# Optimization experiments

Hardware: AMD Instinct MI355X
Metric: run time of the kernel (lower is better)

The kernel has to match this reference:

```python
import jax, jax.numpy as jnp
import numpy as np

NUM_HEADS = 16


def setup_inputs() -> dict:
    key = jax.random.key(0)
    k1, k2, k3, k4 = jax.random.split(key, 4)
    B, N, C = 4, 2048, 1024
    x = jax.random.normal(k1, (B, N, C), dtype=jnp.float32)
    g_info = jax.random.normal(k2, (2, 4, C), dtype=jnp.float32)
    qkv_w = jax.random.normal(k3, (3 * C, C), dtype=jnp.float32) * 0.02
    proj_w = jax.random.normal(k4, (C, C), dtype=jnp.float32) * 0.02
    proj_b = jnp.zeros((C,), dtype=jnp.float32)
    return {"x": x, "g_info": g_info, "qkv_w": qkv_w, "proj_w": proj_w, "proj_b": proj_b}


def reference(x, g_info, qkv_w, proj_w, proj_b):
    B, N, C = x.shape
    H = NUM_HEADS
    D = C // H
    scale = D ** -0.5
    # qkv projection (no bias): [B,N,3C] -> [B,N,3,H,D]
    qkv = (x @ qkv_w.T).reshape(B, N, 3, H, D)
    q, k, v = qkv[:, :, 0], qkv[:, :, 1], qkv[:, :, 2]  # each [B,N,H,D]
    # global-info fusion: g_info[0] -> (4,H,D); rows = q_g, k_g, v_g, t_g
    gl = g_info[0].reshape(4, H, D)
    q_g = gl[0][None, None]  # [1,1,H,D]
    k_g = gl[1][None, None]
    # NOTE: source computes min/max rescaled q_g/k_g but they are dead code;
    # the attention actually uses the unscaled additive fusion below.
    q_fused = q + q_g
    k_fused = k + k_g
    # memory_efficient_attention(q,k,v): softmax(q k^T / sqrt(D)) v
    attn = jnp.einsum("bqhd,bkhd->bhqk", q_fused, k_fused) * scale
    attn = jax.nn.softmax(attn, axis=-1)
    out = jnp.einsum("bhqk,bkhd->bqhd", attn, v).reshape(B, N, C)
    out = out @ proj_w.T + proj_b
    return (out, g_info[1:])
```

## Files before the change

### kernel.cpp

```cpp
#include <hip/hip_runtime.h>

typedef _Float16 h4 __attribute__((ext_vector_type(4)));
typedef _Float16 h8 __attribute__((ext_vector_type(8)));
typedef __fp16 fp16x2 __attribute__((ext_vector_type(2)));
typedef float f4 __attribute__((ext_vector_type(4)));
typedef float f16v __attribute__((ext_vector_type(16)));

#define MFMA16(a,b,c) __builtin_amdgcn_mfma_f32_16x16x32_f16(a, b, c, 0, 0, 0)
#define MFMA32(a,b,c) __builtin_amdgcn_mfma_f32_32x32x16_f16(a, b, c, 0, 0, 0)
#define EXP2(x) __builtin_amdgcn_exp2f(x)

__device__ __forceinline__ void gload_lds16(const _Float16* g, _Float16* l) {
    __builtin_amdgcn_global_load_lds((const __attribute__((address_space(1))) void*)g,
                                     (__attribute__((address_space(3))) void*)l, 16, 0, 0);
}

__device__ __forceinline__ h8 ldfrag_sw(const _Float16* S, int R, int kk, int kq) {
    int b = kk * 4 + (kq >> 1);
    int o = (kq & 1) * 4;
    const _Float16* base = S + R * 64;
    h4 lo = *(const h4*)(base + ((b ^ (R & 7)) * 8) + o);
    h4 hi = *(const h4*)(base + (((b + 2) ^ (R & 7)) * 8) + o);
    return __builtin_shufflevector(lo, hi, 0, 1, 2, 3, 4, 5, 6, 7);
}

__device__ __forceinline__ void gemm_main(const _Float16* __restrict__ A, const _Float16* __restrict__ B,
                                          int K, int tM, int tN, int tid,
                                          _Float16* As, _Float16* Bs, f4 acc[4][4]) {
    int lane = tid & 63, w = tid >> 6;
    int wm = w >> 1, wn = w & 1;
    int ln = lane & 15, kq = lane >> 4;
    int r = tid >> 3;
    int sb = tid & 7;

    for (int k0 = 0; k0 < K; k0 += 64) {
#pragma unroll
        for (int it = 0; it < 4; ++it) {
            int row = r + it * 32;
            int srcb = sb ^ (row & 7);
            const _Float16* ga = A + (size_t)(tM * 128 + row) * K + k0 + srcb * 8;
            const _Float16* gb = B + (size_t)(tN * 128 + row) * K + k0 + srcb * 8;
            _Float16* la = As + ((tid & ~63) + it * 256) * 8;
            _Float16* lb = Bs + ((tid & ~63) + it * 256) * 8;
            gload_lds16(ga, la);
            gload_lds16(gb, lb);
        }
        __syncthreads();
#pragma unroll
        for (int kk = 0; kk < 2; ++kk) {
            h8 af[4], bf[4];
#pragma unroll
            for (int mi = 0; mi < 4; ++mi) af[mi] = ldfrag_sw(As, wm * 64 + mi * 16 + ln, kk, kq);
#pragma unroll
            for (int ni = 0; ni < 4; ++ni) bf[ni] = ldfrag_sw(Bs, wn * 64 + ni * 16 + ln, kk, kq);
#pragma unroll
            for (int mi = 0; mi < 4; ++mi)
#pragma unroll
                for (int ni = 0; ni < 4; ++ni) acc[mi][ni] = MFMA16(af[mi], bf[ni], acc[mi][ni]);
        }
        __syncthreads();
    }
}

__global__ __launch_bounds__(256) void k_cvt(const float* __restrict__ in, _Float16* __restrict__ out, int n8) {
    int stride = gridDim.x * blockDim.x;
    for (int i = blockIdx.x * blockDim.x + threadIdx.x; i < n8; i += stride) {
        float4 a = ((const float4*)in)[i * 2];
        float4 b = ((const float4*)in)[i * 2 + 1];
        h8 r = {(_Float16)a.x, (_Float16)a.y, (_Float16)a.z, (_Float16)a.w,
                (_Float16)b.x, (_Float16)b.y, (_Float16)b.z, (_Float16)b.w};
        ((h8*)out)[i] = r;
    }
}

__global__ __launch_bounds__(256) void k_qkv(const _Float16* __restrict__ A, const _Float16* __restrict__ B,
                                             const float* __restrict__ g, _Float16* __restrict__ Qf,
                                             _Float16* __restrict__ Kf, _Float16* __restrict__ Vt) {
    __shared__ __align__(16) _Float16 As[128 * 64];
    __shared__ __align__(16) _Float16 Bs[128 * 64];
    int tid = threadIdx.x;
    int tN = blockIdx.x, tM = blockIdx.y;
    int lane = tid & 63, w = tid >> 6;
    int wm = w >> 1, wn = w & 1;
    int ln = lane & 15, kq = lane >> 4;

    f4 acc[4][4] = {};
    gemm_main(A, B, 1024, tM, tN, tid, As, Bs, acc);

#pragma unroll
    for (int mi = 0; mi < 4; ++mi) {
#pragma unroll
        for (int ni = 0; ni < 4; ++ni) {
#pragma unroll
            for (int r = 0; r < 4; ++r) {
                int gr = tM * 128 + wm * 64 + mi * 16 + kq * 4 + r;
                int gc = tN * 128 + wn * 64 + ni * 16 + ln;
                float val = acc[mi][ni][r];
                int which = gc >> 10;
                int c = gc & 1023, h = c >> 6, d = c & 63;
                int b = gr >> 11, n = gr & 2047;
                int bh = b * 16 + h;
                if (which == 0) {
                    val += g[c];
                    Qf[((size_t)bh * 2048 + n) * 64 + d] = (_Float16)val;
                } else if (which == 1) {
                    val += g[1024 + c];
                    Kf[((size_t)bh * 2048 + n) * 64 + d] = (_Float16)val;
                } else {
                    Vt[((size_t)bh * 64 + d) * 2048 + n] = (_Float16)val;
                }
            }
        }
    }
}

__global__ __launch_bounds__(256) void k_attn(const _Float16* __restrict__ Qf, const _Float16* __restrict__ Kf,
                                              const _Float16* __restrict__ Vt, _Float16* __restrict__ Oa) {
    __shared__ __align__(16) _Float16 Kl[64 * 64];
    __shared__ __align__(16) _Float16 Vl[64 * 64];
    int tid = threadIdx.x;
    int qt = blockIdx.x, bh = blockIdx.y;
    int lane = tid & 63, w = tid >> 6;
    int l31 = lane & 31, hi = lane >> 5;
    const _Float16* Qb = Qf + (size_t)bh * 2048 * 64;
    const _Float16* Kb = Kf + (size_t)bh * 2048 * 64;
    const _Float16* Vb = Vt + (size_t)bh * 64 * 2048;
    int qrow0 = qt * 128 + w * 32;

    h8 qfr[4];
#pragma unroll
    for (int dc = 0; dc < 4; ++dc) {
        h8 t = *(const h8*)(Qb + (size_t)(qrow0 + l31) * 64 + dc * 16 + hi * 8);
#pragma unroll
        for (int j = 0; j < 8; ++j) t[j] = (_Float16)((float)t[j] * 0.18033688f);
        qfr[dc] = t;
    }

    f16v o0 = {}, o1 = {};
    float m_run = -1e30f, l_run = 0.f;

    for (int kv0 = 0; kv0 < 2048; kv0 += 64) {
#pragma unroll
        for (int it = 0; it < 2; ++it) {
            int slot = tid + it * 256;
            int row = slot >> 3, blk = slot & 7;
            int sb = (blk ^ (row & 7)) * 8;
            *(uint4*)&Kl[row * 64 + sb] = *(const uint4*)(Kb + (size_t)(kv0 + row) * 64 + blk * 8);
            *(uint4*)&Vl[row * 64 + sb] = *(const uint4*)(Vb + (size_t)row * 2048 + kv0 + blk * 8);
        }
        __syncthreads();

        f16v s0 = {}, s1 = {};
        int sw = l31 & 7;
#pragma unroll
        for (int dc = 0; dc < 4; ++dc) {
            int cb = dc * 2 + hi;
            h8 kf0 = *(const h8*)&Kl[l31 * 64 + ((cb ^ sw) * 8)];
            h8 kf1 = *(const h8*)&Kl[(32 + l31) * 64 + ((cb ^ sw) * 8)];
            s0 = MFMA32(kf0, qfr[dc], s0);
            s1 = MFMA32(kf1, qfr[dc], s1);
        }

        float pmax = -1e30f;
#pragma unroll
        for (int r = 0; r < 16; ++r) pmax = fmaxf(pmax, fmaxf(s0[r], s1[r]));
        pmax = fmaxf(pmax, __shfl_xor(pmax, 32, 64));

        bool ok = (pmax <= m_run + 11.5f);
        if (!__all(ok)) {
            float mnew = fmaxf(m_run, pmax);
            float alpha = EXP2(m_run - mnew);
            m_run = mnew;
            l_run *= alpha;
#pragma unroll
            for (int r = 0; r < 16; ++r) {
                int src = (r & 3) + 8 * (r >> 2) + 4 * hi;
                float a = __shfl(alpha, src, 64);
                o0[r] *= a;
                o1[r] *= a;
            }
        }

        float ps0[16], ps1[16];
        float psum = 0.f;
#pragma unroll
        for (int r = 0; r < 16; ++r) { ps0[r] = EXP2(s0[r] - m_run); psum += ps0[r]; }
#pragma unroll
        for (int r = 0; r < 16; ++r) { ps1[r] = EXP2(s1[r] - m_run); psum += ps1[r]; }
        psum += __shfl_xor(psum, 32, 64);
        l_run += psum;

        unsigned W[16];
#pragma unroll
        for (int i = 0; i < 8; ++i) {
            union { fp16x2 h; unsigned u; } a, b;
            a.h = __builtin_amdgcn_cvt_pkrtz(ps0[2 * i], ps0[2 * i + 1]);
            b.h = __builtin_amdgcn_cvt_pkrtz(ps1[2 * i], ps1[2 * i + 1]);
            W[i] = a.u;
            W[8 + i] = b.u;
        }

#pragma unroll
        for (int t = 0; t < 2; ++t) {
#pragma unroll
            for (int kcl = 0; kcl < 2; ++kcl) {
                unsigned w0 = W[t * 8 + kcl * 4 + 0], w1 = W[t * 8 + kcl * 4 + 1];
                unsigned w2 = W[t * 8 + kcl * 4 + 2], w3 = W[t * 8 + kcl * 4 + 3];
                asm("v_permlane32_swap_b32 %0, %1" : "+v"(w0), "+v"(w2));
                asm("v_permlane32_swap_b32 %0, %1" : "+v"(w1), "+v"(w3));
                union { unsigned u[4]; h8 v; } pf;
                pf.u[0] = w0; pf.u[1] = w1; pf.u[2] = w2; pf.u[3] = w3;
                int cb = (t * 2 + kcl) * 2 + hi;
                h8 vf0 = *(const h8*)&Vl[l31 * 64 + ((cb ^ sw) * 8)];
                h8 vf1 = *(const h8*)&Vl[(32 + l31) * 64 + ((cb ^ sw) * 8)];
                o0 = MFMA32(pf.v, vf0, o0);
                o1 = MFMA32(pf.v, vf1, o1);
            }
        }
        __syncthreads();
    }

    float inv = 1.f / l_run;
    int b = bh >> 4, h = bh & 15;
#pragma unroll
    for (int r = 0; r < 16; ++r) {
        int qloc = (r & 3) + 8 * (r >> 2) + 4 * hi;
        float iv = __shfl(inv, qloc, 64);
        size_t base = ((size_t)b * 2048 + qrow0 + qloc) * 1024 + h * 64;
        Oa[base + l31] = (_Float16)(o0[r] * iv);
        Oa[base + 32 + l31] = (_Float16)(o1[r] * iv);
    }
}

__global__ __launch_bounds__(256) void k_proj(const _Float16* __restrict__ A, const _Float16* __restrict__ B,
                                              const float* __restrict__ bias, float* __restrict__ out) {
    __shared__ __align__(16) _Float16 As[128 * 64];
    __shared__ __align__(16) _Float16 Bs[128 * 64];
    int tid = threadIdx.x;
    int tN = blockIdx.x, tM = blockIdx.y;
    int lane = tid & 63, w = tid >> 6;
    int wm = w >> 1, wn = w & 1;
    int ln = lane & 15, kq = lane >> 4;

    f4 acc[4][4] = {};
    gemm_main(A, B, 1024, tM, tN, tid, As, Bs, acc);

#pragma unroll
    for (int mi = 0; mi < 4; ++mi) {
#pragma unroll
        for (int ni = 0; ni < 4; ++ni) {
#pragma unroll
            for (int r = 0; r < 4; ++r) {
                int gr = tM * 128 + wm * 64 + mi * 16 + kq * 4 + r;
                int gc = tN * 128 + wn * 64 + ni * 16 + ln;
                out[(size_t)gr * 1024 + gc] = acc[mi][ni][r] + bias[gc];
            }
        }
    }
}

__global__ __launch_bounds__(256) void k_tail(const float* __restrict__ g, float* __restrict__ out) {
    int i = blockIdx.x * 256 + threadIdx.x;
    out[i] = g[4096 + i];
}

extern "C" void kernel_launch(void* const* d_in, const int* in_sizes, int n_in,
                              void* d_out, int out_size, void* d_ws, size_t ws_size,
                              hipStream_t stream) {
    const float* x = (const float*)d_in[0];
    const float* g = (const float*)d_in[1];
    const float* wq = (const float*)d_in[2];
    const float* wp = (const float*)d_in[3];
    const float* pb = (const float*)d_in[4];
    float* out = (float*)d_out;

    _Float16* xh = (_Float16*)d_ws;
    _Float16* wqh = xh + 8388608;
    _Float16* wph = wqh + 3145728;
    _Float16* Qf = wph + 1048576;
    _Float16* Kf = Qf + 8388608;
    _Float16* Vt = Kf + 8388608;
    _Float16* Oa = xh;

    k_cvt<<<2048, 256, 0, stream>>>(x, xh, 8388608 / 8);
    k_cvt<<<1536, 256, 0, stream>>>(wq, wqh, 3145728 / 8);
    k_cvt<<<512, 256, 0, stream>>>(wp, wph, 1048576 / 8);
    k_qkv<<<dim3(24, 64), 256, 0, stream>>>(xh, wqh, g, Qf, Kf, Vt);
    k_attn<<<dim3(16, 64), 256, 0, stream>>>(Qf, Kf, Vt, Oa);
    k_proj<<<dim3(8, 64), 256, 0, stream>>>(Oa, wph, pb, out);
    k_tail<<<16, 256, 0, stream>>>(g, out + 8388608);
}
```

Baseline: 249.0 us.

## Double-buffer K/V tiles via async global-to-LDS loads in attention

The attention kernel now double-buffers the K and V tiles in shared memory, using direct global-to-LDS loads to prefetch the next KV block while the current one is computed. This removes one barrier per iteration and hides load latency. The Q softmax scale is moved into the QKV GEMM epilogue, the cross-half shuffles are replaced with permlane32 swaps, and MFMA sections are wrapped in s_setprio. Shared memory use doubles, which may lower occupancy.

New measurement: 245.3 us. About the same (-1.5%).

```diff
diff --git a/kernel.cpp b/kernel.cpp
--- a/kernel.cpp
+++ b/kernel.cpp
@@ -13,6 +13,12 @@
 __device__ __forceinline__ void gload_lds16(const _Float16* g, _Float16* l) {
     __builtin_amdgcn_global_load_lds((const __attribute__((address_space(1))) void*)g,
                                      (__attribute__((address_space(3))) void*)l, 16, 0, 0);
+}
+
+__device__ __forceinline__ void half_swap(float v, float& a, float& b) {
+    unsigned x = __float_as_uint(v), y = x;
+    asm("v_permlane32_swap_b32 %0, %1" : "+v"(x), "+v"(y));
+    a = __uint_as_float(x); b = __uint_as_float(y);
 }
 
 __device__ __forceinline__ h8 ldfrag_sw(const _Float16* S, int R, int kk, int kq) {
@@ -101,7 +107,7 @@
                 int b = gr >> 11, n = gr & 2047;
                 int bh = b * 16 + h;
                 if (which == 0) {
-                    val += g[c];
+                    val = (val + g[c]) * 0.18033688f;
                     Qf[((size_t)bh * 2048 + n) * 64 + d] = (_Float16)val;
                 } else if (which == 1) {
                     val += g[1024 + c];
@@ -116,8 +122,7 @@
 
 __global__ __launch_bounds__(256) void k_attn(const _Float16* __restrict__ Qf, const _Float16* __restrict__ Kf,
                                               const _Float16* __restrict__ Vt, _Float16* __restrict__ Oa) {
-    __shared__ __align__(16) _Float16 Kl[64 * 64];
-    __shared__ __align__(16) _Float16 Vl[64 * 64];
+    __shared__ __align__(16) _Float16 KV[2][2][64 * 64];
     int tid = threadIdx.x;
     int qt = blockIdx.x, bh = blockIdx.y;
     int lane = tid & 63, w = tid >> 6;
@@ -127,44 +132,59 @@
     const _Float16* Vb = Vt + (size_t)bh * 64 * 2048;
     int qrow0 = qt * 128 + w * 32;
 
+    int srow = tid >> 3, sblk = tid & 7;
+    int sblk0 = (sblk ^ (srow & 7)) * 8;
+    _Float16* ldst0 = &KV[0][0][0] + (size_t)((tid & ~63)) * 8;
+
+#define STAGE(bufi, kvc)                                                                     \
+    {                                                                                        \
+        _Float16* lk = &KV[bufi][0][0] + ((tid & ~63)) * 8;                                  \
+        _Float16* lv = &KV[bufi][1][0] + ((tid & ~63)) * 8;                                  \
+        gload_lds16(Kb + (size_t)((kvc) + srow) * 64 + sblk0, lk);                           \
+        gload_lds16(Kb + (size_t)((kvc) + srow + 32) * 64 + sblk0, lk + 2048);               \
+        gload_lds16(Vb + (size_t)srow * 2048 + (kvc) + sblk0, lv);                           \
+        gload_lds16(Vb + (size_t)(srow + 32) * 2048 + (kvc) + sblk0, lv + 2048);             \
+    }
+
     h8 qfr[4];
 #pragma unroll
-    for (int dc = 0; dc < 4; ++dc) {
-        h8 t = *(const h8*)(Qb + (size_t)(qrow0 + l31) * 64 + dc * 16 + hi * 8);
-#pragma unroll
-        for (int j = 0; j < 8; ++j) t[j] = (_Float16)((float)t[j] * 0.18033688f);
-        qfr[dc] = t;
-    }
+    for (int dc = 0; dc < 4; ++dc)
+        qfr[dc] = *(const h8*)(Qb + (size_t)(qrow0 + l31) * 64 + dc * 16 + hi * 8);
 
     f16v o0 = {}, o1 = {};
     float m_run = -1e30f, l_run = 0.f;
 
-    for (int kv0 = 0; kv0 < 2048; kv0 += 64) {
-#pragma unroll
-        for (int it = 0; it < 2; ++it) {
-            int slot = tid + it * 256;
-            int row = slot >> 3, blk = slot & 7;
-            int sb = (blk ^ (row & 7)) * 8;
-            *(uint4*)&Kl[row * 64 + sb] = *(const uint4*)(Kb + (size_t)(kv0 + row) * 64 + blk * 8);
-            *(uint4*)&Vl[row * 64 + sb] = *(const uint4*)(Vb + (size_t)row * 2048 + kv0 + blk * 8);
-        }
-        __syncthreads();
+    STAGE(0, 0);
+    __syncthreads();
+
+    int cur = 0;
+    for (int kvc = 0; kvc < 2048; kvc += 64) {
+        if (kvc + 64 < 2048) STAGE(cur ^ 1, kvc + 64);
+
+        const _Float16* Klc = &KV[cur][0][0];
+        const _Float16* Vlc = &KV[cur][1][0];
+        int sw = l31 & 7;
 
         f16v s0 = {}, s1 = {};
-        int sw = l31 & 7;
+        __builtin_amdgcn_s_setprio(1);
 #pragma unroll
         for (int dc = 0; dc < 4; ++dc) {
             int cb = dc * 2 + hi;
-            h8 kf0 = *(const h8*)&Kl[l31 * 64 + ((cb ^ sw) * 8)];
-            h8 kf1 = *(const h8*)&Kl[(32 + l31) * 64 + ((cb ^ sw) * 8)];
+            h8 kf0 = *(const h8*)&Klc[l31 * 64 + ((cb ^ sw) * 8)];
+            h8 kf1 = *(const h8*)&Klc[(32 + l31) * 64 + ((cb ^ sw) * 8)];
             s0 = MFMA32(kf0, qfr[dc], s0);
             s1 = MFMA32(kf1, qfr[dc], s1);
         }
+        __builtin_amdgcn_s_setprio(0);
 
         float pmax = -1e30f;
 #pragma unroll
         for (int r = 0; r < 16; ++r) pmax = fmaxf(pmax, fmaxf(s0[r], s1[r]));
-        pmax = fmaxf(pmax, __shfl_xor(pmax, 32, 64));
+        {
+            float a, b;
+            half_swap(pmax, a, b);
+            pmax = fmaxf(a, b);
+        }
 
         bool ok = (pmax <= m_run + 11.5f);
         if (!__all(ok)) {
@@ -187,7 +207,11 @@
         for (int r = 0; r < 16; ++r) { ps0[r] = EXP2(s0[r] - m_run); psum += ps0[r]; }
 #pragma unroll
         for (int r = 0; r < 16; ++r) { ps1[r] = EXP2(s1[r] - m_run); psum += ps1[r]; }
-        psum += __shfl_xor(psum, 32, 64);
+        {
+            float a, b;
+            half_swap(psum, a, b);
+            psum = a + b;
+        }
         l_run += psum;
 
         unsigned W[16];
@@ -200,6 +224,7 @@
             W[8 + i] = b.u;
         }
 
+        __builtin_amdgcn_s_setprio(1);
 #pragma unroll
         for (int t = 0; t < 2; ++t) {
 #pragma unroll
@@ -211,14 +236,18 @@
                 union { unsigned u[4]; h8 v; } pf;
                 pf.u[0] = w0; pf.u[1] = w1; pf.u[2] = w2; pf.u[3] = w3;
                 int cb = (t * 2 + kcl) * 2 + hi;
-                h8 vf0 = *(const h8*)&Vl[l31 * 64 + ((cb ^ sw) * 8)];
-                h8 vf1 = *(const h8*)&Vl[(32 + l31) * 64 + ((cb ^ sw) * 8)];
+                h8 vf0 = *(const h8*)&Vlc[l31 * 64 + ((cb ^ sw) * 8)];
+                h8 vf1 = *(const h8*)&Vlc[(32 + l31) * 64 + ((cb ^ sw) * 8)];
                 o0 = MFMA32(pf.v, vf0, o0);
                 o1 = MFMA32(pf.v, vf1, o1);
             }
         }
+        __builtin_amdgcn_s_setprio(0);
+
         __syncthreads();
-    }
+        cur ^= 1;
+    }
+#undef STAGE
 
     float inv = 1.f / l_run;
     int b = bh >> 4, h = bh & 15;
```
